# Optimization experiments

Measured on AMD Instinct MI355X. Metric: run time of the kernel, lower is better.

## Reference

```python
import jax, jax.numpy as jnp
import numpy as np
from jax import lax

PATCH = 32  # enc conv kernel/stride
EPS = 1e-12  # F.normalize eps


def setup_inputs() -> dict:
    key = jax.random.key(0)
    ks = jax.random.split(key, 7)
    B, N, H, W = 32, 256, 32, 32
    fdim, vdim = 512, 128
    x = jax.random.normal(ks[0], (B, 3 * N, H, W), dtype=jnp.float32)
    conv_w = jax.random.normal(ks[1], (fdim, 3, PATCH, PATCH), dtype=jnp.float32) * (1.0 / np.sqrt(3 * PATCH * PATCH))
    conv_b = jax.random.normal(ks[2], (fdim,), dtype=jnp.float32) * 0.01
    fc1_w = jax.random.normal(ks[3], (vdim, fdim), dtype=jnp.float32) * (1.0 / np.sqrt(fdim))
    fc1_b = jax.random.normal(ks[4], (vdim,), dtype=jnp.float32) * 0.01
    # deterministic dropout masks (p=0.5, train mode -> keep * 1/(1-p))
    drop1 = (jax.random.uniform(ks[5], (B, N, N)) >= 0.5).astype(jnp.float32) * 2.0
    drop2 = (jax.random.uniform(ks[6], (B, N, N)) >= 0.5).astype(jnp.float32) * 2.0
    return {"x": x, "conv_w": conv_w, "conv_b": conv_b,
            "fc1_w": fc1_w, "fc1_b": fc1_b, "drop1": drop1, "drop2": drop2}


def _branch(scores, drop, eye):
    # softmax over dim=-2, zero diag, dropout, L1-normalize over dim=-2
    P = jax.nn.softmax(scores, axis=-2)
    P = P * (1.0 - eye)
    P = P * drop
    denom = jnp.maximum(jnp.sum(jnp.abs(P), axis=-2, keepdims=True), EPS)
    return P / denom


def reference(x, conv_w, conv_b, fc1_w, fc1_b, drop1, drop2):
    B, C, H, W = x.shape
    N = C // 3
    xi = x.reshape(B * N, 3, H, W)
    # enc: patchify conv -> (B*N, fdim, 1, 1)
    fm = lax.conv_general_dilated(xi, conv_w, (PATCH, PATCH), 'VALID',
                                  dimension_numbers=('NCHW', 'OIHW', 'NCHW'))
    fm = fm + conv_b[None, :, None, None]
    # map2vec: adaptive avgpool(1,1) + flatten + fc1
    v = fm.mean(axis=(2, 3))                      # (B*N, fdim)
    v = v @ fc1_w.T + fc1_b                       # (B*N, vdim)
    f = v.reshape(B, N, -1)                       # (B, N, vdim)
    f_norm = f / jnp.maximum(jnp.linalg.norm(f, axis=-1, keepdims=True), EPS)
    A = jnp.einsum('bnd,bmd->bnm', f_norm, f_norm)  # cosine affinity (B,N,N)
    Atemp = A * (128.0 ** 0.5)                    # torch.div(A, 1/128**0.5)
    eye = jnp.eye(N, dtype=A.dtype)
    A1 = _branch(Atemp, drop1, eye)
    A2t = _branch(jnp.swapaxes(Atemp, -1, -2), drop2, eye)
    AtA = jnp.swapaxes(jnp.matmul(A2t, A1), -1, -2)
    # nll_loss(AtA, arange targets) == -mean of diagonal entries
    diag = jnp.einsum('bii->bi', AtA)
    loss = -jnp.mean(diag)
    return f, A, loss
```

## Files before the change

### kernel.cpp

```cpp
#include <hip/hip_runtime.h>
#include <stdint.h>

#define S_SCALE 11.313708498984761f
#define EPS 1e-12f

typedef __bf16 bf16x8 __attribute__((ext_vector_type(8)));
typedef float  f32x4  __attribute__((ext_vector_type(4)));

__device__ __forceinline__ f32x4 mfma16(bf16x8 a, bf16x8 b, f32x4 c) {
  return __builtin_amdgcn_mfma_f32_16x16x32_bf16(a, b, c, 0, 0, 0);
}

__device__ __forceinline__ float waveSum(float v) {
#pragma unroll
  for (int m = 32; m > 0; m >>= 1) v += __shfl_xor(v, m, 64);
  return v;
}

__device__ __forceinline__ void load_lds16(const float* g, float* l) {
  __builtin_amdgcn_global_load_lds(
      (const __attribute__((address_space(1))) uint32_t*)g,
      (__attribute__((address_space(3))) uint32_t*)l, 16, 0, 0);
}

#define OFF_W    0
#define OFF_BIAS 786432
#define OFF_FN   786944
#define OFF_ZP   2884096

__global__ __launch_bounds__(256) void k_prep(const float* __restrict__ conv_w,
                                              const float* __restrict__ fc1_w,
                                              const float* __restrict__ conv_b,
                                              const float* __restrict__ fc1_b,
                                              __bf16* __restrict__ W,
                                              float* __restrict__ bias2,
                                              float* __restrict__ loss) {
  __shared__ float cw_s[64][36];
  __shared__ float fc1_s[64][65];
  __shared__ float red[4];
  const int t = threadIdx.x;
  if (blockIdx.x >= 192) {
    const int o = blockIdx.x - 192;
    if (o == 0 && t == 0) loss[0] = 0.f;
    float p = fc1_w[o * 512 + t] * conv_b[t] +
              fc1_w[o * 512 + 256 + t] * conv_b[256 + t];
    p = waveSum(p);
    if ((t & 63) == 0) red[t >> 6] = p;
    __syncthreads();
    if (t == 0) bias2[o] = red[0] + red[1] + red[2] + red[3] + fc1_b[o];
    return;
  }
  const int oh = blockIdx.x & 1;
  const int kt = blockIdx.x >> 1;
  const int k0 = kt * 32, o0 = oh * 64;
  const int og = t >> 3, kg = t & 7;
  float acc[2][4] = {};
  for (int cs = 0; cs < 8; ++cs) {
    const int cc = cs * 64;
    __syncthreads();
#pragma unroll
    for (int i = 0; i < 8; ++i) {
      int idx = t + 256 * i;
      int cr = idx >> 5, kk = idx & 31;
      cw_s[cr][kk] = conv_w[(cc + cr) * 3072 + k0 + kk];
    }
#pragma unroll
    for (int i = 0; i < 4; ++i) {
      int idx = t + 256 * i;
      int o = idx >> 4, c4 = (idx & 15) * 4;
      float4 v = *(const float4*)&fc1_w[(o0 + o) * 512 + cc + c4];
      fc1_s[o][c4 + 0] = v.x; fc1_s[o][c4 + 1] = v.y;
      fc1_s[o][c4 + 2] = v.z; fc1_s[o][c4 + 3] = v.w;
    }
    __syncthreads();
    for (int ci = 0; ci < 64; ++ci) {
      float4 cw = *(const float4*)&cw_s[ci][kg * 4];
#pragma unroll
      for (int j = 0; j < 2; ++j) {
        float fv = fc1_s[og * 2 + j][ci];
        acc[j][0] = fmaf(fv, cw.x, acc[j][0]);
        acc[j][1] = fmaf(fv, cw.y, acc[j][1]);
        acc[j][2] = fmaf(fv, cw.z, acc[j][2]);
        acc[j][3] = fmaf(fv, cw.w, acc[j][3]);
      }
    }
  }
#pragma unroll
  for (int j = 0; j < 2; ++j)
#pragma unroll
    for (int q = 0; q < 4; ++q)
      W[(o0 + og * 2 + j) * 3072 + k0 + kg * 4 + q] = (__bf16)acc[j][q];
}

__device__ __forceinline__ void computeTile16(const float* __restrict__ Abuf,
                                              const uint4 (&breg)[2][2],
                                              int l15, int quad,
                                              f32x4 (&acc)[2]) {
  const int rb = l15 * 64;
#pragma unroll
  for (int ks = 0; ks < 2; ++ks) {
    float4 lo = *(const float4*)&Abuf[rb + (((ks * 8 + quad * 2 + 0) ^ l15) << 2)];
    float4 hi = *(const float4*)&Abuf[rb + (((ks * 8 + quad * 2 + 1) ^ l15) << 2)];
    union { __bf16 h[8]; bf16x8 v; } pk;
    pk.h[0] = (__bf16)lo.x; pk.h[1] = (__bf16)lo.y;
    pk.h[2] = (__bf16)lo.z; pk.h[3] = (__bf16)lo.w;
    pk.h[4] = (__bf16)hi.x; pk.h[5] = (__bf16)hi.y;
    pk.h[6] = (__bf16)hi.z; pk.h[7] = (__bf16)hi.w;
    bf16x8 af = pk.v;
#pragma unroll
    for (int ni = 0; ni < 2; ++ni)
      acc[ni] = mfma16(af, *(const bf16x8*)&breg[ks][ni], acc[ni]);
  }
}

__global__ __launch_bounds__(256, 2) void k_gemm1f(const float* __restrict__ x,
                                                   const __bf16* __restrict__ W,
                                                   const float* __restrict__ bias2,
                                                   float* __restrict__ f,
                                                   __bf16* __restrict__ fn) {
  __shared__ __align__(16) float A_lds[2][4][1024];
  __shared__ float rsum[16][5];
  __shared__ float rinv[16];
  const int t = threadIdx.x;
  const int wave = t >> 6, lane = t & 63;
  const int l15 = lane & 15, quad = lane >> 4;
  const int m0 = blockIdx.x * 16;
  const int dr = wave * 4 + (lane >> 4);
  const int dc = ((lane & 15) ^ (dr & 15)) * 4;
  const float* xrow = x + (m0 + dr) * 3072 + dc;
  const __bf16* bp = W + (wave * 32 + l15) * 3072 + quad * 8;

  f32x4 acc[2] = {{0.f, 0.f, 0.f, 0.f}, {0.f, 0.f, 0.f, 0.f}};
  uint4 bX[4][2][2], bY[4][2][2];

  auto burstD = [&](int S, int half) {
#pragma unroll
    for (int i = 0; i < 4; ++i)
      load_lds16(xrow + S * 256 + i * 64, &A_lds[half][i][wave * 256]);
  };
  auto loadB4 = [&](int S, uint4(&d)[4][2][2]) {
#pragma unroll
    for (int i = 0; i < 4; ++i)
#pragma unroll
      for (int ks = 0; ks < 2; ++ks)
#pragma unroll
        for (int ni = 0; ni < 2; ++ni)
          d[i][ks][ni] =
              *(const uint4*)(bp + ni * 16 * 3072 + S * 256 + i * 64 + ks * 32);
  };
  auto compute4 = [&](int half, const uint4(&d)[4][2][2]) {
#pragma unroll
    for (int i = 0; i < 4; ++i)
      computeTile16(&A_lds[half][i][0], d[i], l15, quad, acc);
  };

  burstD(0, 0);
  loadB4(0, bX);
  __syncthreads();

  for (int s2 = 0; s2 < 6; ++s2) {
    const int S0 = s2 * 2;
    burstD(S0 + 1, 1);
    loadB4(S0 + 1, bY);
    __builtin_amdgcn_sched_barrier(0);
    compute4(0, bX);
    __syncthreads();
    if (s2 < 5) {
      burstD(S0 + 2, 0);
      loadB4(S0 + 2, bX);
    }
    __builtin_amdgcn_sched_barrier(0);
    compute4(1, bY);
    __syncthreads();
  }

  const float b0 = bias2[wave * 32 + l15];
  const float b1 = bias2[wave * 32 + 16 + l15];
#pragma unroll
  for (int r = 0; r < 4; ++r) {
    acc[0][r] += b0;
    acc[1][r] += b1;
    float s = acc[0][r] * acc[0][r] + acc[1][r] * acc[1][r];
    s += __shfl_xor(s, 1, 64);
    s += __shfl_xor(s, 2, 64);
    s += __shfl_xor(s, 4, 64);
    s += __shfl_xor(s, 8, 64);
    if (l15 == 0) rsum[quad * 4 + r][wave] = s;
  }
  __syncthreads();
  if (t < 16) {
    float s = rsum[t][0] + rsum[t][1] + rsum[t][2] + rsum[t][3];
    rinv[t] = 1.f / fmaxf(sqrtf(s), EPS);
  }
  __syncthreads();
#pragma unroll
  for (int r = 0; r < 4; ++r) {
    const int row = quad * 4 + r;
    const float iv = rinv[row];
    const int g = (m0 + row) * 128 + wave * 32 + l15;
    f[g] = acc[0][r];
    fn[g] = (__bf16)(acc[0][r] * iv);
    f[g + 16] = acc[1][r];
    fn[g + 16] = (__bf16)(acc[1][r] * iv);
  }
}

__global__ __launch_bounds__(256) void k_gemm2(const __bf16* __restrict__ fn,
                                               const float* __restrict__ d1,
                                               const float* __restrict__ d2,
                                               float* __restrict__ Aout,
                                               float* __restrict__ Zp) {
  __shared__ __align__(16) __bf16 Li[64][136];
  __shared__ __align__(16) __bf16 Lj[64][136];
  __shared__ float zred[2][4][64];
  const int t = threadIdx.x;
  const int b = blockIdx.y;
  const int ti = blockIdx.x >> 2, tj = blockIdx.x & 3;
  const int i0 = ti * 64, j0 = tj * 64;
  const int wave = t >> 6, lane = t & 63;
  const int l15 = lane & 15, quad = lane >> 4;
  const __bf16* fb = fn + b * 32768;
#pragma unroll
  for (int i = 0; i < 4; ++i) {
    int idx = t + 256 * i;
    int r = idx >> 4, c8 = (idx & 15) * 8;
    *(uint4*)&Li[r][c8] = *(const uint4*)&fb[(i0 + r) * 128 + c8];
    *(uint4*)&Lj[r][c8] = *(const uint4*)&fb[(j0 + r) * 128 + c8];
  }
  __syncthreads();
  f32x4 acc[4] = {{0.f, 0.f, 0.f, 0.f}, {0.f, 0.f, 0.f, 0.f},
                  {0.f, 0.f, 0.f, 0.f}, {0.f, 0.f, 0.f, 0.f}};
#pragma unroll
  for (int ks = 0; ks < 4; ++ks) {
    bf16x8 af = *(const bf16x8*)&Li[wave * 16 + l15][ks * 32 + quad * 8];
#pragma unroll
    for (int nt = 0; nt < 4; ++nt) {
      bf16x8 bf = *(const bf16x8*)&Lj[nt * 16 + l15][ks * 32 + quad * 8];
      acc[nt] = mfma16(af, bf, acc[nt]);
    }
  }
  const int base = b * 65536;
  float* Ab = Aout + base;
  float z1c[4] = {0.f, 0.f, 0.f, 0.f}, z2c[4] = {0.f, 0.f, 0.f, 0.f};
#pragma unroll
  for (int nt = 0; nt < 4; ++nt) {
    int gj = j0 + nt * 16 + l15;
#pragma unroll
    for (int r = 0; r < 4; ++r) {
      int gi = i0 + wave * 16 + quad * 4 + r;
      float a = acc[nt][r];
      Ab[gi * 256 + gj] = a;
      float e = __expf(fmaf(S_SCALE, a, -S_SCALE));
      if (gi != gj) {
        int idx = base + gi * 256 + gj;
        z1c[nt] = fmaf(e, d1[idx], z1c[nt]);
        z2c[nt] = fmaf(e, d2[idx], z2c[nt]);
      }
    }
  }
#pragma unroll
  for (int nt = 0; nt < 4; ++nt) {
    z1c[nt] += __shfl_xor(z1c[nt], 16, 64);
    z1c[nt] += __shfl_xor(z1c[nt], 32, 64);
    z2c[nt] += __shfl_xor(z2c[nt], 16, 64);
    z2c[nt] += __shfl_xor(z2c[nt], 32, 64);
  }
  if (quad == 0) {
#pragma unroll
    for (int nt = 0; nt < 4; ++nt) {
      zred[0][wave][nt * 16 + l15] = z1c[nt];
      zred[1][wave][nt * 16 + l15] = z2c[nt];
    }
  }
  __syncthreads();
  if (t < 128) {
    int z = t >> 6, c = t & 63;
    float s = zred[z][0][c] + zred[z][1][c] + zred[z][2][c] + zred[z][3][c];
    Zp[(z * 4 + ti) * 8192 + b * 256 + j0 + c] = s;
  }
}

__global__ __launch_bounds__(256) void k_loss(const float* __restrict__ Aout,
                                              const float* __restrict__ d1,
                                              const float* __restrict__ d2,
                                              const float* __restrict__ Zp,
                                              float* __restrict__ loss) {
  __shared__ float d1s[64][65];
  __shared__ float z1s[64], z2s[64];
  __shared__ float red[4];
  const int t = threadIdx.x;
  const int b = blockIdx.y;
  const int ic = blockIdx.x >> 2, kc = blockIdx.x & 3;
  const int i0 = ic * 64, k0 = kc * 64;
  const int base = b * 65536;
  if (t < 64) {
    float s = 0.f;
#pragma unroll
    for (int p = 0; p < 4; ++p) s += Zp[p * 8192 + b * 256 + i0 + t];
    z1s[t] = 1.f / fmaxf(s, EPS);
  } else if (t < 128) {
    float s = 0.f;
#pragma unroll
    for (int p = 0; p < 4; ++p) s += Zp[(4 + p) * 8192 + b * 256 + k0 + t - 64];
    z2s[t - 64] = 1.f / fmaxf(s, EPS);
  }
#pragma unroll
  for (int ii = 0; ii < 16; ++ii) {
    int idx = t + 256 * ii;
    int kr = idx >> 6, ci = idx & 63;
    d1s[kr][ci] = d1[base + (k0 + kr) * 256 + i0 + ci];
  }
  __syncthreads();
  const int kl = t & 63, ig = t >> 6;
  float inv2 = z2s[kl];
  float accv = 0.f;
  for (int ii = 0; ii < 16; ++ii) {
    int il = ig * 16 + ii;
    int idx = base + (i0 + il) * 256 + k0 + kl;
    float a = Aout[idx];
    float e = __expf(fmaf(2.f * S_SCALE, a, -2.f * S_SCALE));
    float v = e * d2[idx] * d1s[kl][il] * z1s[il] * inv2;
    if (i0 + il != k0 + kl) accv += v;
  }
  accv = waveSum(accv);
  if ((t & 63) == 0) red[t >> 6] = accv;
  __syncthreads();
  if (t == 0) {
    float tot = red[0] + red[1] + red[2] + red[3];
    atomicAdd(loss, tot * (-1.f / 8192.f));
  }
}

extern "C" void kernel_launch(void* const* d_in, const int* in_sizes, int n_in,
                              void* d_out, int out_size, void* d_ws,
                              size_t ws_size, hipStream_t stream) {
  const float* x = (const float*)d_in[0];
  const float* conv_w = (const float*)d_in[1];
  const float* conv_b = (const float*)d_in[2];
  const float* fc1_w = (const float*)d_in[3];
  const float* fc1_b = (const float*)d_in[4];
  const float* drop1 = (const float*)d_in[5];
  const float* drop2 = (const float*)d_in[6];
  char* ws = (char*)d_ws;
  __bf16* W = (__bf16*)(ws + OFF_W);
  float* bias2 = (float*)(ws + OFF_BIAS);
  __bf16* fn = (__bf16*)(ws + OFF_FN);
  float* Zp = (float*)(ws + OFF_ZP);
  float* f = (float*)d_out;
  float* Aout = f + 1048576;
  float* loss = f + 3145728;

  k_prep<<<320, 256, 0, stream>>>(conv_w, fc1_w, conv_b, fc1_b, W, bias2, loss);
  k_gemm1f<<<512, 256, 0, stream>>>(x, W, bias2, f, fn);
  k_gemm2<<<dim3(16, 32), 256, 0, stream>>>(fn, drop1, drop2, Aout, Zp);
  k_loss<<<dim3(16, 32), 256, 0, stream>>>(Aout, drop1, drop2, Zp, loss);
}
```

Before: 244.8 us.

## Retile fused patch GEMM to 64-row blocks with 8 waves and wider N tiles

The first GEMM (x times the folded conv/fc weight) now has each block cover 64 rows with 512 threads. Waves form a 4x2 grid and each computes a 16x64 output tile, so each wave issues 4 MFMAs per A fragment. The goal is more reuse of each weight fragment loaded from global memory and fewer redundant weight loads across blocks. The cost is only 128 blocks, which may underfill the GPU's CUs, plus heavier register use for the B buffers.

Result: slower. 301.8 us (+23.3%).

```diff
diff --git a/kernel.cpp b/kernel.cpp
--- a/kernel.cpp
+++ b/kernel.cpp
@@ -92,116 +92,117 @@
       W[(o0 + og * 2 + j) * 3072 + k0 + kg * 4 + q] = (__bf16)acc[j][q];
 }
 
-__device__ __forceinline__ void computeTile16(const float* __restrict__ Abuf,
-                                              const uint4 (&breg)[2][2],
-                                              int l15, int quad,
-                                              f32x4 (&acc)[2]) {
-  const int rb = l15 * 64;
-#pragma unroll
-  for (int ks = 0; ks < 2; ++ks) {
-    float4 lo = *(const float4*)&Abuf[rb + (((ks * 8 + quad * 2 + 0) ^ l15) << 2)];
-    float4 hi = *(const float4*)&Abuf[rb + (((ks * 8 + quad * 2 + 1) ^ l15) << 2)];
-    union { __bf16 h[8]; bf16x8 v; } pk;
-    pk.h[0] = (__bf16)lo.x; pk.h[1] = (__bf16)lo.y;
-    pk.h[2] = (__bf16)lo.z; pk.h[3] = (__bf16)lo.w;
-    pk.h[4] = (__bf16)hi.x; pk.h[5] = (__bf16)hi.y;
-    pk.h[6] = (__bf16)hi.z; pk.h[7] = (__bf16)hi.w;
-    bf16x8 af = pk.v;
-#pragma unroll
-    for (int ni = 0; ni < 2; ++ni)
-      acc[ni] = mfma16(af, *(const bf16x8*)&breg[ks][ni], acc[ni]);
-  }
-}
-
-__global__ __launch_bounds__(256, 2) void k_gemm1f(const float* __restrict__ x,
+__global__ __launch_bounds__(512, 2) void k_gemm1f(const float* __restrict__ x,
                                                    const __bf16* __restrict__ W,
                                                    const float* __restrict__ bias2,
                                                    float* __restrict__ f,
                                                    __bf16* __restrict__ fn) {
-  __shared__ __align__(16) float A_lds[2][4][1024];
-  __shared__ float rsum[16][5];
-  __shared__ float rinv[16];
+  __shared__ __align__(16) float A_lds[2][64 * 128];
+  __shared__ float rsum[64][2];
+  __shared__ float rinv[64];
   const int t = threadIdx.x;
   const int wave = t >> 6, lane = t & 63;
-  const int l15 = lane & 15, quad = lane >> 4;
-  const int m0 = blockIdx.x * 16;
-  const int dr = wave * 4 + (lane >> 4);
-  const int dc = ((lane & 15) ^ (dr & 15)) * 4;
-  const float* xrow = x + (m0 + dr) * 3072 + dc;
-  const __bf16* bp = W + (wave * 32 + l15) * 3072 + quad * 8;
-
-  f32x4 acc[2] = {{0.f, 0.f, 0.f, 0.f}, {0.f, 0.f, 0.f, 0.f}};
-  uint4 bX[4][2][2], bY[4][2][2];
+  const int wm = wave >> 1, wn = wave & 1;
+  const int l15 = lane & 15, quad = (lane >> 4) & 3;
+  const int m0 = blockIdx.x * 64;
+
+  int drows[4], dcols[4];
+#pragma unroll
+  for (int j = 0; j < 4; ++j) {
+    int r = (wave * 4 + j) * 2 + (lane >> 5);
+    int cl = (lane & 31) ^ (r & 15);
+    drows[j] = r;
+    dcols[j] = cl * 4;
+  }
+  const __bf16* bp = W + (wn * 64 + l15) * 3072 + quad * 8;
+
+  f32x4 acc[4] = {{0.f, 0.f, 0.f, 0.f}, {0.f, 0.f, 0.f, 0.f},
+                  {0.f, 0.f, 0.f, 0.f}, {0.f, 0.f, 0.f, 0.f}};
+  uint4 bX[4][4], bY[4][4];
 
   auto burstD = [&](int S, int half) {
 #pragma unroll
-    for (int i = 0; i < 4; ++i)
-      load_lds16(xrow + S * 256 + i * 64, &A_lds[half][i][wave * 256]);
+    for (int j = 0; j < 4; ++j)
+      load_lds16(x + (m0 + drows[j]) * 3072 + S * 128 + dcols[j],
+                 &A_lds[half][(wave * 4 + j) * 256]);
   };
-  auto loadB4 = [&](int S, uint4(&d)[4][2][2]) {
-#pragma unroll
-    for (int i = 0; i < 4; ++i)
-#pragma unroll
-      for (int ks = 0; ks < 2; ++ks)
-#pragma unroll
-        for (int ni = 0; ni < 2; ++ni)
-          d[i][ks][ni] =
-              *(const uint4*)(bp + ni * 16 * 3072 + S * 256 + i * 64 + ks * 32);
+  auto loadB = [&](int S, uint4(&d)[4][4]) {
+#pragma unroll
+    for (int ks = 0; ks < 4; ++ks)
+#pragma unroll
+      for (int ni = 0; ni < 4; ++ni)
+        d[ks][ni] = *(const uint4*)(bp + ni * 16 * 3072 + S * 128 + ks * 32);
   };
-  auto compute4 = [&](int half, const uint4(&d)[4][2][2]) {
-#pragma unroll
-    for (int i = 0; i < 4; ++i)
-      computeTile16(&A_lds[half][i][0], d[i], l15, quad, acc);
+  auto computeB = [&](int half, const uint4(&d)[4][4]) {
+    const float* Abuf = &A_lds[half][0];
+    const int arow = wm * 16 + l15;
+    const int rb = arow * 128;
+#pragma unroll
+    for (int ks = 0; ks < 4; ++ks) {
+      float4 lo = *(const float4*)&Abuf[rb + (((ks * 8 + quad * 2 + 0) ^ l15) << 2)];
+      float4 hi = *(const float4*)&Abuf[rb + (((ks * 8 + quad * 2 + 1) ^ l15) << 2)];
+      union { __bf16 h[8]; bf16x8 v; } pk;
+      pk.h[0] = (__bf16)lo.x; pk.h[1] = (__bf16)lo.y;
+      pk.h[2] = (__bf16)lo.z; pk.h[3] = (__bf16)lo.w;
+      pk.h[4] = (__bf16)hi.x; pk.h[5] = (__bf16)hi.y;
+      pk.h[6] = (__bf16)hi.z; pk.h[7] = (__bf16)hi.w;
+      bf16x8 af = pk.v;
+#pragma unroll
+      for (int ni = 0; ni < 4; ++ni)
+        acc[ni] = mfma16(af, *(const bf16x8*)&d[ks][ni], acc[ni]);
+    }
   };
 
   burstD(0, 0);
-  loadB4(0, bX);
-  __syncthreads();
-
-  for (int s2 = 0; s2 < 6; ++s2) {
+  loadB(0, bX);
+  __syncthreads();
+
+  for (int s2 = 0; s2 < 12; ++s2) {
     const int S0 = s2 * 2;
     burstD(S0 + 1, 1);
-    loadB4(S0 + 1, bY);
+    loadB(S0 + 1, bY);
     __builtin_amdgcn_sched_barrier(0);
-    compute4(0, bX);
-    __syncthreads();
-    if (s2 < 5) {
+    computeB(0, bX);
+    __syncthreads();
+    if (s2 < 11) {
       burstD(S0 + 2, 0);
-      loadB4(S0 + 2, bX);
+      loadB(S0 + 2, bX);
     }
     __builtin_amdgcn_sched_barrier(0);
-    compute4(1, bY);
-    __syncthreads();
-  }
-
-  const float b0 = bias2[wave * 32 + l15];
-  const float b1 = bias2[wave * 32 + 16 + l15];
+    computeB(1, bY);
+    __syncthreads();
+  }
+
+#pragma unroll
+  for (int ni = 0; ni < 4; ++ni) {
+    const float bv = bias2[wn * 64 + ni * 16 + l15];
+#pragma unroll
+    for (int r = 0; r < 4; ++r) acc[ni][r] += bv;
+  }
 #pragma unroll
   for (int r = 0; r < 4; ++r) {
-    acc[0][r] += b0;
-    acc[1][r] += b1;
-    float s = acc[0][r] * acc[0][r] + acc[1][r] * acc[1][r];
+    float s = 0.f;
+#pragma unroll
+    for (int ni = 0; ni < 4; ++ni) s = fmaf(acc[ni][r], acc[ni][r], s);
     s += __shfl_xor(s, 1, 64);
     s += __shfl_xor(s, 2, 64);
     s += __shfl_xor(s, 4, 64);
     s += __shfl_xor(s, 8, 64);
-    if (l15 == 0) rsum[quad * 4 + r][wave] = s;
-  }
-  __syncthreads();
-  if (t < 16) {
-    float s = rsum[t][0] + rsum[t][1] + rsum[t][2] + rsum[t][3];
-    rinv[t] = 1.f / fmaxf(sqrtf(s), EPS);
-  }
+    if (l15 == 0) rsum[wm * 16 + quad * 4 + r][wn] = s;
+  }
+  __syncthreads();
+  if (t < 64) rinv[t] = 1.f / fmaxf(sqrtf(rsum[t][0] + rsum[t][1]), EPS);
   __syncthreads();
 #pragma unroll
   for (int r = 0; r < 4; ++r) {
-    const int row = quad * 4 + r;
+    const int row = wm * 16 + quad * 4 + r;
     const float iv = rinv[row];
-    const int g = (m0 + row) * 128 + wave * 32 + l15;
-    f[g] = acc[0][r];
-    fn[g] = (__bf16)(acc[0][r] * iv);
-    f[g + 16] = acc[1][r];
-    fn[g + 16] = (__bf16)(acc[1][r] * iv);
+#pragma unroll
+    for (int ni = 0; ni < 4; ++ni) {
+      const int g = (m0 + row) * 128 + wn * 64 + ni * 16 + l15;
+      f[g] = acc[ni][r];
+      fn[g] = (__bf16)(acc[ni][r] * iv);
+    }
   }
 }
 
@@ -351,7 +352,7 @@
   float* loss = f + 3145728;
 
   k_prep<<<320, 256, 0, stream>>>(conv_w, fc1_w, conv_b, fc1_b, W, bias2, loss);
-  k_gemm1f<<<512, 256, 0, stream>>>(x, W, bias2, f, fn);
+  k_gemm1f<<<128, 512, 0, stream>>>(x, W, bias2, f, fn);
   k_gemm2<<<dim3(16, 32), 256, 0, stream>>>(fn, drop1, drop2, Aout, Zp);
   k_loss<<<dim3(16, 32), 256, 0, stream>>>(Aout, drop1, drop2, Zp, loss);
 }
```
